# Performance work log

Hardware: AMD Instinct MI355X
Metric: run time of the kernel (lower is better)

Reference implementation:

```python
import jax, jax.numpy as jnp
import numpy as np

D, H, DH = 64, 4, 32
INNER = H * DH
SCALE = 1.0 / np.sqrt(DH)


def _layernorm(x, w, b, eps=1e-5):
    mu = jnp.mean(x, axis=-1, keepdims=True)
    var = jnp.var(x, axis=-1, keepdims=True)
    return (x - mu) * jax.lax.rsqrt(var + eps) * w + b


def setup_inputs() -> dict:
    key = jax.random.key(0)
    ks = jax.random.split(key, 8)
    B, N = 1, 256
    z = jax.random.normal(ks[0], (B, N, N, D), dtype=jnp.float32)
    mask = jax.random.randint(ks[1], (B, N, N), 0, 2).astype(jnp.bool_)
    ln_w = jnp.ones((D,), jnp.float32)
    ln_b = jnp.zeros((D,), jnp.float32)
    w_qkv = jax.random.normal(ks[2], (3 * INNER, D), jnp.float32) * 0.02
    w_bias = jax.random.normal(ks[3], (H, D), jnp.float32) * 0.02
    w_out = jax.random.normal(ks[4], (D, INNER), jnp.float32) * 0.02
    w_gate = jax.random.normal(ks[5], (INNER, D), jnp.float32) * 0.02
    return {"z": z, "mask": mask, "ln_w": ln_w, "ln_b": ln_b,
            "w_qkv": w_qkv, "w_bias": w_bias, "w_out": w_out, "w_gate": w_gate}


def reference(z, mask, ln_w, ln_b, w_qkv, w_bias, w_out, w_gate):
    # mode == 'starting': attend along the second pair axis per row n.
    B, N = z.shape[0], z.shape[1]
    h = _layernorm(z, ln_w, ln_b)                       # [B,N,N,D]
    qkv = jnp.einsum('bijd,ed->bije', h, w_qkv)         # [B,N,N,3*INNER]
    qkv = qkv.reshape(B, N, N, 3, H, DH)
    q, k, v = qkv[..., 0, :, :], qkv[..., 1, :, :], qkv[..., 2, :, :]  # [B,N,N,H,dh]
    attn = jnp.einsum('bnihd,bnjhd->bnhij', q, k) * SCALE  # [B,N,H,N,N]
    bias = jnp.einsum('bijd,hd->bhij', h, w_bias)          # [B,H,N,N]
    attn = attn + bias[:, None]                            # broadcast over n
    big_neg = jnp.finfo(attn.dtype).min
    attn = jnp.where(mask[:, :, None, None, :], attn, big_neg)  # mask keys j per (b,n)
    attn = jax.nn.softmax(attn, axis=-1)
    out = jnp.einsum('bnhij,bnjhd->bnihd', attn, v)        # [B,N,N,H,dh]
    out = out.reshape(B, N, N, INNER)
    gate = jax.nn.sigmoid(jnp.einsum('bijd,ed->bije', h, w_gate))
    out = jnp.einsum('bije,de->bijd', out * gate, w_out)
    return out
```

## Files before the change

### kernel.cpp

```cpp
#include <hip/hip_runtime.h>
#include <hip/hip_bf16.h>

#define N_ 256
#define D_ 64
#define H_ 4
#define DH_ 32
#define EQKV 384
#define NPOS 65536
#define SCALE_F 0.17677669529663687f
#define BIG_NEG -3.402823466e38f
#define P_STRIDE 264
#define H_STRIDE 72
#define X_STRIDE 136
#define A_STRIDE 136
#define O_STRIDE 68
#define Q_STRIDE 392

typedef __attribute__((ext_vector_type(8))) short s16x8;
typedef __attribute__((ext_vector_type(4))) float f32x4;


__device__ inline short bfbits(float x) {
    __hip_bfloat16 b = __float2bfloat16(x);
    return *reinterpret_cast<short*>(&b);
}
__device__ inline float b2f(short s) {
    unsigned u = ((unsigned)(unsigned short)s) << 16;
    union { unsigned u; float f; } c; c.u = u; return c.f;
}
__device__ inline s16x8 cvt8(float4 a, float4 b) {
    s16x8 r;
    r[0] = bfbits(a.x); r[1] = bfbits(a.y); r[2] = bfbits(a.z); r[3] = bfbits(a.w);
    r[4] = bfbits(b.x); r[5] = bfbits(b.y); r[6] = bfbits(b.z); r[7] = bfbits(b.w);
    return r;
}

__global__ __launch_bounds__(512) void k1_ln_proj_mfma(
    const float* __restrict__ z, const float* __restrict__ ln_w, const float* __restrict__ ln_b,
    const float* __restrict__ w_qkv, const float* __restrict__ w_bias,
    __hip_bfloat16* __restrict__ qkv_ws, __hip_bfloat16* __restrict__ h_ws,
    float* __restrict__ bias_ws)
{
    __shared__ __align__(16) short smem[64 * Q_STRIDE];
    const int t = threadIdx.x;
    const int wave = t >> 6, lane = t & 63;
    const int pos0 = blockIdx.x * 64;
    const int m = lane & 15, quad = lane >> 4;

    {
        const int oct = lane >> 3;
        const int ocl = lane & 7;
        const int row = wave * 8 + oct;
        const int d0 = ocl * 8;

        const float* zp = z + (size_t)(pos0 + row) * 64 + d0;
        const float4 z0 = *(const float4*)(zp);
        const float4 z1 = *(const float4*)(zp + 4);

        float s  = z0.x + z0.y + z0.z + z0.w + z1.x + z1.y + z1.z + z1.w;
        float s2 = z0.x*z0.x + z0.y*z0.y + z0.z*z0.z + z0.w*z0.w
                 + z1.x*z1.x + z1.y*z1.y + z1.z*z1.z + z1.w*z1.w;
        #pragma unroll
        for (int off = 1; off < 8; off <<= 1) { s += __shfl_xor(s, off); s2 += __shfl_xor(s2, off); }
        const float mu = s * 0.015625f;
        const float var = s2 * 0.015625f - mu * mu;
        const float rs = rsqrtf(var + 1e-5f);

        const float4 lw0 = *(const float4*)(ln_w + d0);
        const float4 lw1 = *(const float4*)(ln_w + d0 + 4);
        const float4 lb0 = *(const float4*)(ln_b + d0);
        const float4 lb1 = *(const float4*)(ln_b + d0 + 4);

        float hv[8];
        hv[0] = (z0.x - mu) * rs * lw0.x + lb0.x;
        hv[1] = (z0.y - mu) * rs * lw0.y + lb0.y;
        hv[2] = (z0.z - mu) * rs * lw0.z + lb0.z;
        hv[3] = (z0.w - mu) * rs * lw0.w + lb0.w;
        hv[4] = (z1.x - mu) * rs * lw1.x + lb1.x;
        hv[5] = (z1.y - mu) * rs * lw1.y + lb1.y;
        hv[6] = (z1.z - mu) * rs * lw1.z + lb1.z;
        hv[7] = (z1.w - mu) * rs * lw1.w + lb1.w;

        s16x8 hb;
        #pragma unroll
        for (int k = 0; k < 8; ++k) hb[k] = bfbits(hv[k]);
        *(s16x8*)(smem + row * H_STRIDE + d0) = hb;

        float bsum[4];
        #pragma unroll
        for (int h4 = 0; h4 < 4; ++h4) {
            const float4 wb0 = *(const float4*)(w_bias + h4 * 64 + d0);
            const float4 wb1 = *(const float4*)(w_bias + h4 * 64 + d0 + 4);
            float b = hv[0]*wb0.x + hv[1]*wb0.y + hv[2]*wb0.z + hv[3]*wb0.w
                    + hv[4]*wb1.x + hv[5]*wb1.y + hv[6]*wb1.z + hv[7]*wb1.w;
            #pragma unroll
            for (int off = 1; off < 8; off <<= 1) b += __shfl_xor(b, off);
            bsum[h4] = b;
        }
        if (ocl == 0) {
            const int gpos = pos0 + row;
            const int gi = gpos >> 8, gj = gpos & 255;
            #pragma unroll
            for (int h4 = 0; h4 < 4; ++h4)
                bias_ws[h4 * NPOS + gi * 256 + gj] = bsum[h4];
        }
    }
    __syncthreads();

    {
        const int row = t >> 3, c8 = (t & 7) * 8;
        *(s16x8*)(h_ws + (size_t)(pos0 + row) * 64 + c8) =
            *(const s16x8*)(smem + row * H_STRIDE + c8);
    }

    const int colbase = wave * 48;
    s16x8 bfrag[3][2];
    #pragma unroll
    for (int nt = 0; nt < 3; ++nt) {
        const int col = colbase + nt * 16 + m;
        const float* wp = w_qkv + (size_t)col * 64;
        #pragma unroll
        for (int kt = 0; kt < 2; ++kt) {
            const float4 w0 = *(const float4*)(wp + kt * 32 + quad * 8);
            const float4 w1 = *(const float4*)(wp + kt * 32 + quad * 8 + 4);
            bfrag[nt][kt] = cvt8(w0, w1);
        }
    }

    s16x8 afrag[4][2];
    #pragma unroll
    for (int mt = 0; mt < 4; ++mt)
        #pragma unroll
        for (int kt = 0; kt < 2; ++kt)
            afrag[mt][kt] = *(const s16x8*)(smem + (mt * 16 + m) * H_STRIDE + kt * 32 + quad * 8);

    f32x4 acc[4][3];
    #pragma unroll
    for (int mt = 0; mt < 4; ++mt)
        #pragma unroll
        for (int nt = 0; nt < 3; ++nt)
            acc[mt][nt] = (f32x4){0.f, 0.f, 0.f, 0.f};

    #pragma unroll
    for (int kt = 0; kt < 2; ++kt)
        #pragma unroll
        for (int mt = 0; mt < 4; ++mt)
            #pragma unroll
            for (int nt = 0; nt < 3; ++nt)
                acc[mt][nt] = __builtin_amdgcn_mfma_f32_16x16x32_bf16(
                    afrag[mt][kt], bfrag[nt][kt], acc[mt][nt], 0, 0, 0);

    __syncthreads();

    #pragma unroll
    for (int mt = 0; mt < 4; ++mt)
        #pragma unroll
        for (int nt = 0; nt < 3; ++nt) {
            const int c = colbase + nt * 16 + m;
            #pragma unroll
            for (int r = 0; r < 4; ++r) {
                const int row = mt * 16 + quad * 4 + r;
                smem[row * Q_STRIDE + c] = bfbits(acc[mt][nt][r]);
            }
        }
    __syncthreads();

    #pragma unroll
    for (int i = 0; i < 6; ++i) {
        const int idx = i * 512 + t;
        const int row = idx / 48, c8 = (idx % 48) * 8;
        *(s16x8*)(qkv_ws + (size_t)(pos0 + row) * EQKV + c8) =
            *(const s16x8*)(smem + row * Q_STRIDE + c8);
    }
}

__global__ __launch_bounds__(512, 4) void k2_attn_mfma(
    const __hip_bfloat16* __restrict__ qkv_ws, const float* __restrict__ bias_ws,
    const int* __restrict__ mask, __hip_bfloat16* __restrict__ attn_bf)
{
    __shared__ __align__(16) short p_s[64 * P_STRIDE];
    __shared__ __align__(16) short vt_s[32 * P_STRIDE];
    __shared__ float keep[256];
    __shared__ float redl[64][2];

    const int bx = blockIdx.x;
    const int n = bx & 255, h = bx >> 8;
    const int t = threadIdx.x;
    const int wave = t >> 6, lane = t & 63;
    const int m = lane & 15, quad = lane >> 4;
    const int mt = wave & 3, nh = wave >> 2;

    if (t < 256) keep[t] = (mask[n * 256 + t] != 0) ? 1.0f : 0.0f;

    {
        const int j = t >> 1, dh = (t & 1) * 16;
        const __hip_bfloat16* vp = qkv_ws + (size_t)(n * 256 + j) * 384 + 256 + h * 32 + dh;
        s16x8 v0 = *(const s16x8*)vp;
        s16x8 v1 = *(const s16x8*)(vp + 8);
        #pragma unroll
        for (int e = 0; e < 8; ++e) {
            vt_s[(dh + e) * P_STRIDE + j]     = v0[e];
            vt_s[(dh + 8 + e) * P_STRIDE + j] = v1[e];
        }
    }

    s16x8 kf[8];
    #pragma unroll
    for (int tt = 0; tt < 8; ++tt) {
        const int jt = nh * 8 + tt;
        kf[tt] = *(const s16x8*)(qkv_ws + (size_t)(n * 256 + jt * 16 + m) * 384 + 128 + h * 32 + quad * 8);
    }

    const int jcol0 = nh * 128 + m;
    const float* bias_h = bias_ws + (size_t)h * NPOS;
    s16x8 qf = *(const s16x8*)(qkv_ws + (size_t)(n * 256 + mt * 16 + m) * 384 + h * 32 + quad * 8);
    float bb[8][4];
    #pragma unroll
    for (int tt = 0; tt < 8; ++tt)
        #pragma unroll
        for (int r = 0; r < 4; ++r)
            bb[tt][r] = bias_h[(mt * 16 + quad * 4 + r) * 256 + jcol0 + tt * 16];

    __syncthreads();

    for (int ig = 0; ig < 4; ++ig) {
        const int i0 = ig * 64;

        f32x4 s[8];
        #pragma unroll
        for (int tt = 0; tt < 8; ++tt) {
            f32x4 z4 = {0.f, 0.f, 0.f, 0.f};
            s[tt] = __builtin_amdgcn_mfma_f32_16x16x32_bf16(qf, kf[tt], z4, 0, 0, 0);
        }
        #pragma unroll
        for (int tt = 0; tt < 8; ++tt) {
            const float kp = keep[jcol0 + tt * 16];
            #pragma unroll
            for (int r = 0; r < 4; ++r) {
                const float sv = s[tt][r] * SCALE_F + bb[tt][r];
                s[tt][r] = (kp != 0.f) ? sv : BIG_NEG;
            }
        }

        {
            float ls[4];
            #pragma unroll
            for (int r = 0; r < 4; ++r) {
                float acc = 0.f;
                #pragma unroll
                for (int tt = 0; tt < 8; ++tt) {
                    const float p = __expf(s[tt][r]);
                    s[tt][r] = p;
                    acc += p;
                }
                #pragma unroll
                for (int off = 1; off < 16; off <<= 1) acc += __shfl_xor(acc, off);
                ls[r] = acc;
            }
            if (m == 0) {
                #pragma unroll
                for (int r = 0; r < 4; ++r) redl[mt * 16 + quad * 4 + r][nh] = ls[r];
            }
            #pragma unroll
            for (int tt = 0; tt < 8; ++tt) {
                const int col = (nh * 8 + tt) * 16 + m;
                #pragma unroll
                for (int r = 0; r < 4; ++r) {
                    const int row = mt * 16 + quad * 4 + r;
                    p_s[row * P_STRIDE + col] = bfbits(s[tt][r]);
                }
            }
        }

        if (ig < 3) {
            const int i0n = i0 + 64;
            qf = *(const s16x8*)(qkv_ws + (size_t)(n * 256 + i0n + mt * 16 + m) * 384 + h * 32 + quad * 8);
            #pragma unroll
            for (int tt = 0; tt < 8; ++tt)
                #pragma unroll
                for (int r = 0; r < 4; ++r)
                    bb[tt][r] = bias_h[(i0n + mt * 16 + quad * 4 + r) * 256 + jcol0 + tt * 16];
        }
        __syncthreads();

        {
            f32x4 o0 = {0.f, 0.f, 0.f, 0.f};
            f32x4 o1 = {0.f, 0.f, 0.f, 0.f};
            const int arow = mt * 16 + m;
            const int brow = nh * 16 + m;
            #pragma unroll
            for (int kt = 0; kt < 4; ++kt) {
                const s16x8 ap0 = *(const s16x8*)(p_s + arow * P_STRIDE + (2 * kt) * 32 + quad * 8);
                const s16x8 bv0 = *(const s16x8*)(vt_s + brow * P_STRIDE + (2 * kt) * 32 + quad * 8);
                o0 = __builtin_amdgcn_mfma_f32_16x16x32_bf16(ap0, bv0, o0, 0, 0, 0);
                const s16x8 ap1 = *(const s16x8*)(p_s + arow * P_STRIDE + (2 * kt + 1) * 32 + quad * 8);
                const s16x8 bv1 = *(const s16x8*)(vt_s + brow * P_STRIDE + (2 * kt + 1) * 32 + quad * 8);
                o1 = __builtin_amdgcn_mfma_f32_16x16x32_bf16(ap1, bv1, o1, 0, 0, 0);
            }
            #pragma unroll
            for (int r = 0; r < 4; ++r) {
                const int row = mt * 16 + quad * 4 + r;
                const float l = fmaxf(redl[row][0] + redl[row][1], 1e-30f);
                const float val = (o0[r] + o1[r]) * (1.0f / l);
                const int ig_row = i0 + row;
                attn_bf[(size_t)(n * 256 + ig_row) * 128 + h * 32 + nh * 16 + m] = __float2bfloat16(val);
            }
        }
        __syncthreads();
    }
}

__global__ __launch_bounds__(512) void k3_proj_mfma(
    const __hip_bfloat16* __restrict__ attn_bf, const __hip_bfloat16* __restrict__ h_ws,
    const float* __restrict__ w_gate, const float* __restrict__ w_out, float* __restrict__ out)
{
    __shared__ __align__(16) short h_s[64 * H_STRIDE];
    __shared__ __align__(16) short a_s[64 * A_STRIDE];
    __shared__ __align__(16) short x_s[64 * X_STRIDE];
    const int t = threadIdx.x;
    const int wave = t >> 6, lane = t & 63;
    const int pos0 = blockIdx.x * 64;
    const int m = lane & 15, quad = lane >> 4;

    {
        const int row = t >> 3, c8 = (t & 7) * 8;
        *(s16x8*)(h_s + row * H_STRIDE + c8) =
            *(const s16x8*)(h_ws + (size_t)(pos0 + row) * 64 + c8);
    }
    #pragma unroll
    for (int i = 0; i < 2; ++i) {
        const int idx = i * 512 + t;
        const int row = idx >> 4, c8 = (idx & 15) * 8;
        *(s16x8*)(a_s + row * A_STRIDE + c8) =
            *(const s16x8*)(attn_bf + (size_t)(pos0 + row) * 128 + c8);
    }
    __syncthreads();

    {
        const int mt = wave & 3, cg = wave >> 2;
        s16x8 ha[2];
        #pragma unroll
        for (int kt = 0; kt < 2; ++kt)
            ha[kt] = *(const s16x8*)(h_s + (mt * 16 + m) * H_STRIDE + kt * 32 + quad * 8);
        #pragma unroll
        for (int nt = 0; nt < 4; ++nt) {
            const float* wp = w_gate + (size_t)(cg * 64 + nt * 16 + m) * 64;
            const s16x8 b0 = cvt8(*(const float4*)(wp + quad * 8),
                                  *(const float4*)(wp + quad * 8 + 4));
            const s16x8 b1 = cvt8(*(const float4*)(wp + 32 + quad * 8),
                                  *(const float4*)(wp + 32 + quad * 8 + 4));
            f32x4 g4 = (f32x4){0.f, 0.f, 0.f, 0.f};
            g4 = __builtin_amdgcn_mfma_f32_16x16x32_bf16(ha[0], b0, g4, 0, 0, 0);
            g4 = __builtin_amdgcn_mfma_f32_16x16x32_bf16(ha[1], b1, g4, 0, 0, 0);
            const int col = cg * 64 + nt * 16 + m;
            #pragma unroll
            for (int r = 0; r < 4; ++r) {
                const int row = mt * 16 + quad * 4 + r;
                const float gv = 1.0f / (1.0f + __expf(-g4[r]));
                x_s[row * X_STRIDE + col] = bfbits(b2f(a_s[row * A_STRIDE + col]) * gv);
            }
        }
    }
    __syncthreads();

    const int mt = wave & 3, nh = wave >> 2;
    s16x8 bfrag[2][4];
    #pragma unroll
    for (int nt = 0; nt < 2; ++nt) {
        const int d = nh * 32 + nt * 16 + m;
        const float* wp = w_out + (size_t)d * 128;
        #pragma unroll
        for (int kt = 0; kt < 4; ++kt) {
            const float4 w0 = *(const float4*)(wp + kt * 32 + quad * 8);
            const float4 w1 = *(const float4*)(wp + kt * 32 + quad * 8 + 4);
            bfrag[nt][kt] = cvt8(w0, w1);
        }
    }

    s16x8 afrag[4];
    #pragma unroll
    for (int kt = 0; kt < 4; ++kt)
        afrag[kt] = *(const s16x8*)(x_s + (mt * 16 + m) * X_STRIDE + kt * 32 + quad * 8);

    f32x4 acc[2];
    acc[0] = (f32x4){0.f, 0.f, 0.f, 0.f};
    acc[1] = (f32x4){0.f, 0.f, 0.f, 0.f};
    #pragma unroll
    for (int kt = 0; kt < 4; ++kt) {
        acc[0] = __builtin_amdgcn_mfma_f32_16x16x32_bf16(afrag[kt], bfrag[0][kt], acc[0], 0, 0, 0);
        acc[1] = __builtin_amdgcn_mfma_f32_16x16x32_bf16(afrag[kt], bfrag[1][kt], acc[1], 0, 0, 0);
    }

    float* o_s = (float*)a_s;
    #pragma unroll
    for (int nt = 0; nt < 2; ++nt) {
        const int d = nh * 32 + nt * 16 + m;
        #pragma unroll
        for (int r = 0; r < 4; ++r) {
            const int row = mt * 16 + quad * 4 + r;
            o_s[row * O_STRIDE + d] = acc[nt][r];
        }
    }
    __syncthreads();

    #pragma unroll
    for (int i = 0; i < 2; ++i) {
        const int idx = i * 512 + t;
        const int row = idx >> 4, c4 = (idx & 15) * 4;
        *(float4*)(out + (size_t)(pos0 + row) * 64 + c4) =
            *(const float4*)(o_s + row * O_STRIDE + c4);
    }
}

extern "C" void kernel_launch(void* const* d_in, const int* in_sizes, int n_in,
                              void* d_out, int out_size, void* d_ws, size_t ws_size,
                              hipStream_t stream) {
    const float* z      = (const float*)d_in[0];
    const int*   mask   = (const int*)d_in[1];
    const float* ln_w   = (const float*)d_in[2];
    const float* ln_b   = (const float*)d_in[3];
    const float* w_qkv  = (const float*)d_in[4];
    const float* w_bias = (const float*)d_in[5];
    const float* w_out  = (const float*)d_in[6];
    const float* w_gate = (const float*)d_in[7];
    float* out = (float*)d_out;

    char* ws = (char*)d_ws;
    __hip_bfloat16* qkv_ws  = (__hip_bfloat16*)(ws);
    float*          bias_ws = (float*)(ws + 50331648);
    __hip_bfloat16* h_ws    = (__hip_bfloat16*)(ws + 51380224);
    __hip_bfloat16* attn_bf = (__hip_bfloat16*)(ws + 59768832);

    k1_ln_proj_mfma<<<1024, 512, 0, stream>>>(z, ln_w, ln_b, w_qkv, w_bias,
                                              qkv_ws, h_ws, bias_ws);
    k2_attn_mfma<<<1024, 512, 0, stream>>>(qkv_ws, bias_ws, mask, attn_bf);
    k3_proj_mfma<<<1024, 512, 0, stream>>>(attn_bf, h_ws, w_gate, w_out, out);
}
```

Measured before the change: 177.6 us.

## Fuse gate projection and sigmoid into the LN/QKV kernel, drop h workspace

The gate projection moves from the final kernel into the first one. The QKV GEMM is widened from 384 to 512 output columns, and the sigmoid gate is computed there and stored to a new fp32 workspace, so the bf16 normalized-activation workspace is no longer needed. The final kernel now builds its MFMA A-fragments directly from global attention output times the precomputed gate, with no LDS staging and no gate GEMM. The cost is a 32MB fp32 gate tensor written and read instead of an 8MB bf16 h tensor. The first kernel also gains a launch-bounds occupancy hint, and its LDS gate buffer uses a 130-float stride that leaves float4 reads misaligned on odd rows.

Result: slower. 190.5 us (+7.2%).

```diff
diff --git a/kernel.cpp b/kernel.cpp
--- a/kernel.cpp
+++ b/kernel.cpp
@@ -6,15 +6,15 @@
 #define H_ 4
 #define DH_ 32
 #define EQKV 384
+#define EGATE 128
 #define NPOS 65536
 #define SCALE_F 0.17677669529663687f
 #define BIG_NEG -3.402823466e38f
 #define P_STRIDE 264
 #define H_STRIDE 72
-#define X_STRIDE 136
-#define A_STRIDE 136
 #define O_STRIDE 68
 #define Q_STRIDE 392
+#define G_STRIDE 130
 
 typedef __attribute__((ext_vector_type(8))) short s16x8;
 typedef __attribute__((ext_vector_type(4))) float f32x4;
@@ -35,11 +35,10 @@
     return r;
 }
 
-__global__ __launch_bounds__(512) void k1_ln_proj_mfma(
+__global__ __launch_bounds__(512, 2) void k1_ln_proj_mfma(
     const float* __restrict__ z, const float* __restrict__ ln_w, const float* __restrict__ ln_b,
-    const float* __restrict__ w_qkv, const float* __restrict__ w_bias,
-    __hip_bfloat16* __restrict__ qkv_ws, __hip_bfloat16* __restrict__ h_ws,
-    float* __restrict__ bias_ws)
+    const float* __restrict__ w_qkv, const float* __restrict__ w_gate, const float* __restrict__ w_bias,
+    __hip_bfloat16* __restrict__ qkv_ws, float* __restrict__ gate_ws, float* __restrict__ bias_ws)
 {
     __shared__ __align__(16) short smem[64 * Q_STRIDE];
     const int t = threadIdx.x;
@@ -107,18 +106,13 @@
     }
     __syncthreads();
 
-    {
-        const int row = t >> 3, c8 = (t & 7) * 8;
-        *(s16x8*)(h_ws + (size_t)(pos0 + row) * 64 + c8) =
-            *(const s16x8*)(smem + row * H_STRIDE + c8);
-    }
-
-    const int colbase = wave * 48;
-    s16x8 bfrag[3][2];
-    #pragma unroll
-    for (int nt = 0; nt < 3; ++nt) {
+    const int colbase = wave * 64;
+    s16x8 bfrag[4][2];
+    #pragma unroll
+    for (int nt = 0; nt < 4; ++nt) {
         const int col = colbase + nt * 16 + m;
-        const float* wp = w_qkv + (size_t)col * 64;
+        const float* wp = (col < EQKV) ? (w_qkv + (size_t)col * 64)
+                                       : (w_gate + (size_t)(col - EQKV) * 64);
         #pragma unroll
         for (int kt = 0; kt < 2; ++kt) {
             const float4 w0 = *(const float4*)(wp + kt * 32 + quad * 8);
@@ -134,11 +128,11 @@
         for (int kt = 0; kt < 2; ++kt)
             afrag[mt][kt] = *(const s16x8*)(smem + (mt * 16 + m) * H_STRIDE + kt * 32 + quad * 8);
 
-    f32x4 acc[4][3];
+    f32x4 acc[4][4];
     #pragma unroll
     for (int mt = 0; mt < 4; ++mt)
         #pragma unroll
-        for (int nt = 0; nt < 3; ++nt)
+        for (int nt = 0; nt < 4; ++nt)
             acc[mt][nt] = (f32x4){0.f, 0.f, 0.f, 0.f};
 
     #pragma unroll
@@ -146,23 +140,25 @@
         #pragma unroll
         for (int mt = 0; mt < 4; ++mt)
             #pragma unroll
-            for (int nt = 0; nt < 3; ++nt)
+            for (int nt = 0; nt < 4; ++nt)
                 acc[mt][nt] = __builtin_amdgcn_mfma_f32_16x16x32_bf16(
                     afrag[mt][kt], bfrag[nt][kt], acc[mt][nt], 0, 0, 0);
 
     __syncthreads();
 
-    #pragma unroll
-    for (int mt = 0; mt < 4; ++mt)
-        #pragma unroll
-        for (int nt = 0; nt < 3; ++nt) {
-            const int c = colbase + nt * 16 + m;
-            #pragma unroll
-            for (int r = 0; r < 4; ++r) {
-                const int row = mt * 16 + quad * 4 + r;
-                smem[row * Q_STRIDE + c] = bfbits(acc[mt][nt][r]);
-            }
-        }
+    if (colbase < EQKV) {
+        #pragma unroll
+        for (int mt = 0; mt < 4; ++mt)
+            #pragma unroll
+            for (int nt = 0; nt < 4; ++nt) {
+                const int c = colbase + nt * 16 + m;
+                #pragma unroll
+                for (int r = 0; r < 4; ++r) {
+                    const int row = mt * 16 + quad * 4 + r;
+                    smem[row * Q_STRIDE + c] = bfbits(acc[mt][nt][r]);
+                }
+            }
+    }
     __syncthreads();
 
     #pragma unroll
@@ -171,6 +167,35 @@
         const int row = idx / 48, c8 = (idx % 48) * 8;
         *(s16x8*)(qkv_ws + (size_t)(pos0 + row) * EQKV + c8) =
             *(const s16x8*)(smem + row * Q_STRIDE + c8);
+    }
+    __syncthreads();
+
+    if (colbase >= EQKV) {
+        float* gf = (float*)smem;
+        const int gb = colbase - EQKV;
+        #pragma unroll
+        for (int mt = 0; mt < 4; ++mt)
+            #pragma unroll
+            for (int nt = 0; nt < 4; ++nt) {
+                const int gc = gb + nt * 16 + m;
+                #pragma unroll
+                for (int r = 0; r < 4; ++r) {
+                    const int row = mt * 16 + quad * 4 + r;
+                    gf[row * G_STRIDE + gc] = 1.0f / (1.0f + __expf(-acc[mt][nt][r]));
+                }
+            }
+    }
+    __syncthreads();
+
+    {
+        const float* gf = (const float*)smem;
+        #pragma unroll
+        for (int i = 0; i < 4; ++i) {
+            const int idx = i * 512 + t;
+            const int row = idx >> 5, c4 = (idx & 31) * 4;
+            *(float4*)(gate_ws + (size_t)(pos0 + row) * EGATE + c4) =
+                *(const float4*)(gf + row * G_STRIDE + c4);
+        }
     }
 }
 
@@ -311,59 +336,31 @@
 }
 
 __global__ __launch_bounds__(512) void k3_proj_mfma(
-    const __hip_bfloat16* __restrict__ attn_bf, const __hip_bfloat16* __restrict__ h_ws,
-    const float* __restrict__ w_gate, const float* __restrict__ w_out, float* __restrict__ out)
+    const __hip_bfloat16* __restrict__ attn_bf, const float* __restrict__ gate_ws,
+    const float* __restrict__ w_out, float* __restrict__ out)
 {
-    __shared__ __align__(16) short h_s[64 * H_STRIDE];
-    __shared__ __align__(16) short a_s[64 * A_STRIDE];
-    __shared__ __align__(16) short x_s[64 * X_STRIDE];
+    __shared__ __align__(16) float o_s[64 * O_STRIDE];
     const int t = threadIdx.x;
     const int wave = t >> 6, lane = t & 63;
     const int pos0 = blockIdx.x * 64;
     const int m = lane & 15, quad = lane >> 4;
-
-    {
-        const int row = t >> 3, c8 = (t & 7) * 8;
-        *(s16x8*)(h_s + row * H_STRIDE + c8) =
-            *(const s16x8*)(h_ws + (size_t)(pos0 + row) * 64 + c8);
-    }
-    #pragma unroll
-    for (int i = 0; i < 2; ++i) {
-        const int idx = i * 512 + t;
-        const int row = idx >> 4, c8 = (idx & 15) * 8;
-        *(s16x8*)(a_s + row * A_STRIDE + c8) =
-            *(const s16x8*)(attn_bf + (size_t)(pos0 + row) * 128 + c8);
-    }
-    __syncthreads();
-
-    {
-        const int mt = wave & 3, cg = wave >> 2;
-        s16x8 ha[2];
-        #pragma unroll
-        for (int kt = 0; kt < 2; ++kt)
-            ha[kt] = *(const s16x8*)(h_s + (mt * 16 + m) * H_STRIDE + kt * 32 + quad * 8);
-        #pragma unroll
-        for (int nt = 0; nt < 4; ++nt) {
-            const float* wp = w_gate + (size_t)(cg * 64 + nt * 16 + m) * 64;
-            const s16x8 b0 = cvt8(*(const float4*)(wp + quad * 8),
-                                  *(const float4*)(wp + quad * 8 + 4));
-            const s16x8 b1 = cvt8(*(const float4*)(wp + 32 + quad * 8),
-                                  *(const float4*)(wp + 32 + quad * 8 + 4));
-            f32x4 g4 = (f32x4){0.f, 0.f, 0.f, 0.f};
-            g4 = __builtin_amdgcn_mfma_f32_16x16x32_bf16(ha[0], b0, g4, 0, 0, 0);
-            g4 = __builtin_amdgcn_mfma_f32_16x16x32_bf16(ha[1], b1, g4, 0, 0, 0);
-            const int col = cg * 64 + nt * 16 + m;
-            #pragma unroll
-            for (int r = 0; r < 4; ++r) {
-                const int row = mt * 16 + quad * 4 + r;
-                const float gv = 1.0f / (1.0f + __expf(-g4[r]));
-                x_s[row * X_STRIDE + col] = bfbits(b2f(a_s[row * A_STRIDE + col]) * gv);
-            }
-        }
-    }
-    __syncthreads();
-
     const int mt = wave & 3, nh = wave >> 2;
+
+    s16x8 afrag[4];
+    #pragma unroll
+    for (int kt = 0; kt < 4; ++kt) {
+        const size_t g = (size_t)(pos0 + mt * 16 + m) * 128 + kt * 32 + quad * 8;
+        const s16x8 a8 = *(const s16x8*)(attn_bf + g);
+        const float4 g0 = *(const float4*)(gate_ws + g);
+        const float4 g1 = *(const float4*)(gate_ws + g + 4);
+        s16x8 x8;
+        x8[0] = bfbits(b2f(a8[0]) * g0.x); x8[1] = bfbits(b2f(a8[1]) * g0.y);
+        x8[2] = bfbits(b2f(a8[2]) * g0.z); x8[3] = bfbits(b2f(a8[3]) * g0.w);
+        x8[4] = bfbits(b2f(a8[4]) * g1.x); x8[5] = bfbits(b2f(a8[5]) * g1.y);
+        x8[6] = bfbits(b2f(a8[6]) * g1.z); x8[7] = bfbits(b2f(a8[7]) * g1.w);
+        afrag[kt] = x8;
+    }
+
     s16x8 bfrag[2][4];
     #pragma unroll
     for (int nt = 0; nt < 2; ++nt) {
@@ -377,11 +374,6 @@
         }
     }
 
-    s16x8 afrag[4];
-    #pragma unroll
-    for (int kt = 0; kt < 4; ++kt)
-        afrag[kt] = *(const s16x8*)(x_s + (mt * 16 + m) * X_STRIDE + kt * 32 + quad * 8);
-
     f32x4 acc[2];
     acc[0] = (f32x4){0.f, 0.f, 0.f, 0.f};
     acc[1] = (f32x4){0.f, 0.f, 0.f, 0.f};
@@ -391,7 +383,6 @@
         acc[1] = __builtin_amdgcn_mfma_f32_16x16x32_bf16(afrag[kt], bfrag[1][kt], acc[1], 0, 0, 0);
     }
 
-    float* o_s = (float*)a_s;
     #pragma unroll
     for (int nt = 0; nt < 2; ++nt) {
         const int d = nh * 32 + nt * 16 + m;
@@ -428,11 +419,11 @@
     char* ws = (char*)d_ws;
     __hip_bfloat16* qkv_ws  = (__hip_bfloat16*)(ws);
     float*          bias_ws = (float*)(ws + 50331648);
-    __hip_bfloat16* h_ws    = (__hip_bfloat16*)(ws + 51380224);
-    __hip_bfloat16* attn_bf = (__hip_bfloat16*)(ws + 59768832);
-
-    k1_ln_proj_mfma<<<1024, 512, 0, stream>>>(z, ln_w, ln_b, w_qkv, w_bias,
-                                              qkv_ws, h_ws, bias_ws);
+    float*          gate_ws = (float*)(ws + 51380224);
+    __hip_bfloat16* attn_bf = (__hip_bfloat16*)(ws + 84934656);
+
+    k1_ln_proj_mfma<<<1024, 512, 0, stream>>>(z, ln_w, ln_b, w_qkv, w_gate, w_bias,
+                                              qkv_ws, gate_ws, bias_ws);
     k2_attn_mfma<<<1024, 512, 0, stream>>>(qkv_ws, bias_ws, mask, attn_bf);
-    k3_proj_mfma<<<1024, 512, 0, stream>>>(attn_bf, h_ws, w_gate, w_out, out);
-}
+    k3_proj_mfma<<<1024, 512, 0, stream>>>(attn_bf, gate_ws, w_out, out);
+}
```
